# Optimization experiments

Hardware: AMD Instinct MI355X
Metric: run time of the kernel (lower is better)

## Reference

```python
import jax, jax.numpy as jnp
import numpy as np

N, E, IN, H, C = 50000, 800000, 256, 4, 64  # nodes, edges, input_dim, heads, hidden_dim


def setup_inputs() -> dict:
    key = jax.random.key(0)
    ks = jax.random.split(key, 12)
    rn = lambda k, shp, s: jax.random.normal(k, shp, jnp.float32) * s
    glorot = lambda fi, fo: (2.0 / (fi + fo)) ** 0.5
    return {
        "x": rn(ks[0], (N, IN), 1.0),
        "edge_index": jax.random.randint(ks[1], (2, E), 0, N, dtype=jnp.int32),
        # gat1: in=IN, out=H*C, concat=True
        "W1": rn(ks[2], (IN, H * C), glorot(IN, H * C)),
        "att_src1": rn(ks[3], (H, C), 0.1),
        "att_dst1": rn(ks[4], (H, C), 0.1),
        "b1": jnp.zeros((H * C,), jnp.float32),
        # gat2: in=H*C, out=C, heads=1, concat=False
        "W2": rn(ks[5], (H * C, C), glorot(H * C, C)),
        "att_src2": rn(ks[6], (1, C), 0.1),
        "att_dst2": rn(ks[7], (1, C), 0.1),
        "b2": jnp.zeros((C,), jnp.float32),
        # attention pooling head + entity scorer
        "att_w": rn(ks[8], (C, 1), 0.1),
        "att_b": jnp.zeros((1,), jnp.float32),
        "fc_w": rn(ks[9], (C, 1), 0.1),
        "fc_b": jnp.zeros((1,), jnp.float32),
    }


def _gat_conv(x, src, dst, W, a_src, a_dst, bias, concat):
    """PyG GATConv (self-loops already appended to src/dst)."""
    n = x.shape[0]
    heads, ch = a_src.shape
    h = (x @ W).reshape(n, heads, ch)                      # [N,H,C]
    s = jnp.sum(h * a_src[None], axis=-1)                  # [N,H]
    d = jnp.sum(h * a_dst[None], axis=-1)                  # [N,H]
    e = jax.nn.leaky_relu(s[src] + d[dst], 0.2)            # [Etot,H]
    # segment softmax over incoming edges of each dst node
    m = jax.ops.segment_max(e, dst, num_segments=n)        # [N,H]
    m = jnp.where(jnp.isfinite(m), m, 0.0)
    ex = jnp.exp(e - m[dst])
    den = jax.ops.segment_sum(ex, dst, num_segments=n)
    alpha = ex / den[dst]                                  # [Etot,H]
    out = jax.ops.segment_sum(h[src] * alpha[:, :, None], dst, num_segments=n)  # [N,H,C]
    out = out.reshape(n, heads * ch) if concat else out.mean(axis=1)
    return out + bias


def reference(x, edge_index, W1, att_src1, att_dst1, b1, W2, att_src2, att_dst2, b2,
              att_w, att_b, fc_w, fc_b):
    n = x.shape[0]
    loop = jnp.arange(n, dtype=edge_index.dtype)           # add_self_loops=True
    src = jnp.concatenate([edge_index[0], loop])
    dst = jnp.concatenate([edge_index[1], loop])
    h = jax.nn.relu(_gat_conv(x, src, dst, W1, att_src1, att_dst1, b1, True))   # [N,H*C]
    h = jax.nn.relu(_gat_conv(h, src, dst, W2, att_src2, att_dst2, b2, False))  # [N,C]
    aw = jax.nn.softmax(h @ att_w + att_b, axis=0)         # softmax over all nodes, [N,1]
    global_rep = jnp.sum(aw * h, axis=0)                   # [C]
    entity_probs = jax.nn.sigmoid(h @ fc_w + fc_b).squeeze(-1)  # [N]
    return entity_probs, global_rep
```

## Files before the change

### kernel.cpp

```cpp
#include <hip/hip_runtime.h>
#include <hip/hip_bf16.h>
#include <math.h>

#define N_NODES 50000
#define N_EDGES 800000
#define ETOT    850000
#define IN_DIM  256
#define HC      256
#define HEADS   4
#define CD      64

typedef __bf16    bf16x8 __attribute__((ext_vector_type(8)));
typedef float     f32x4  __attribute__((ext_vector_type(4)));
typedef _Float16  f16x4  __attribute__((ext_vector_type(4)));

static __device__ __forceinline__ float lrelu(float x) { return x > 0.f ? x : 0.2f * x; }

static __device__ __forceinline__ unsigned short bf16_rne(float f) {
    union { float f; unsigned u; } c; c.f = f;
    unsigned u = c.u;
    return (unsigned short)((u + 0x7FFFu + ((u >> 16) & 1u)) >> 16);
}
static __device__ __forceinline__ float bf16_to_f(unsigned short h) {
    union { unsigned u; float f; } c; c.u = ((unsigned)h) << 16;
    return c.f;
}

__global__ void k_init(int* counts, int* cursor,
                       float* s1, float* d1, float* s2, float* d2) {
    int i = blockIdx.x * 256 + threadIdx.x;
    if (i < N_NODES) {
        counts[i] = 1; cursor[i] = 0;
        float4 z = {0.f, 0.f, 0.f, 0.f};
        reinterpret_cast<float4*>(s1)[i] = z;
        reinterpret_cast<float4*>(d1)[i] = z;
        s2[i] = 0.f; d2[i] = 0.f;
    }
}

__global__ void k_degree(const int* __restrict__ dst, int* __restrict__ counts) {
    int i = blockIdx.x * 256 + threadIdx.x;
    if (i < N_EDGES) atomicAdd(&counts[dst[i]], 1);
}

__global__ __launch_bounds__(1024) void k_scan_a(const int* __restrict__ counts,
                                                 int* __restrict__ rowptr,
                                                 int* __restrict__ bsum) {
    __shared__ int sd[1024];
    int t = threadIdx.x;
    int i = blockIdx.x * 1024 + t;
    int v = (i < N_NODES) ? counts[i] : 0;
    sd[t] = v; __syncthreads();
    for (int off = 1; off < 1024; off <<= 1) {
        int add = (t >= off) ? sd[t - off] : 0;
        __syncthreads();
        sd[t] += add;
        __syncthreads();
    }
    if (i < N_NODES) rowptr[i + 1] = sd[t];
    if (t == 1023) bsum[blockIdx.x] = sd[1023];
    if (i == 0) rowptr[0] = 0;
}

__global__ void k_scan_b(int* bsum, int nb) {
    if (threadIdx.x == 0) {
        int run = 0;
        for (int b = 0; b < nb; ++b) { int t = bsum[b]; bsum[b] = run; run += t; }
    }
}

__global__ void k_scan_c(int* __restrict__ rowptr, const int* __restrict__ bsum) {
    int i = blockIdx.x * 256 + threadIdx.x;
    if (i < N_NODES) rowptr[i + 1] += bsum[i >> 10];
}

__global__ void k_scatter(const int* __restrict__ src, const int* __restrict__ dst,
                          const int* __restrict__ rowptr, int* __restrict__ cursor,
                          int* __restrict__ src_sorted) {
    int i = blockIdx.x * 256 + threadIdx.x;
    if (i >= ETOT) return;
    int s, d;
    if (i < N_EDGES) { s = src[i]; d = dst[i]; }
    else             { s = i - N_EDGES; d = s; }
    int pos = rowptr[d] + atomicAdd(&cursor[d], 1);
    src_sorted[pos] = s;
}

__global__ void k_convx(const float* __restrict__ x,
                        unsigned short* __restrict__ hi,
                        unsigned short* __restrict__ lo) {
    int i = blockIdx.x * 256 + threadIdx.x;
    if (i >= N_NODES * IN_DIM / 4) return;
    float4 v = reinterpret_cast<const float4*>(x)[i];
    ushort4 h, l;
    h.x = bf16_rne(v.x); l.x = bf16_rne(v.x - bf16_to_f(h.x));
    h.y = bf16_rne(v.y); l.y = bf16_rne(v.y - bf16_to_f(h.y));
    h.z = bf16_rne(v.z); l.z = bf16_rne(v.z - bf16_to_f(h.z));
    h.w = bf16_rne(v.w); l.w = bf16_rne(v.w - bf16_to_f(h.w));
    reinterpret_cast<ushort4*>(hi)[i] = h;
    reinterpret_cast<ushort4*>(lo)[i] = l;
}

__global__ void k_convw(const float* __restrict__ W,
                        unsigned short* __restrict__ hiT,
                        unsigned short* __restrict__ loT, int Nc) {
    int idx = blockIdx.x * 256 + threadIdx.x;
    if (idx >= Nc * 256) return;
    int n = idx >> 8, k = idx & 255;
    float v = W[(size_t)k * Nc + n];
    unsigned short h = bf16_rne(v);
    hiT[idx] = h;
    loT[idx] = bf16_rne(v - bf16_to_f(h));
}

__global__ __launch_bounds__(256) void k_gemm_f(
    const unsigned short* __restrict__ Ahi, const unsigned short* __restrict__ Alo,
    const unsigned short* __restrict__ BThi, const unsigned short* __restrict__ BTlo,
    _Float16* __restrict__ Of16,
    float* __restrict__ s_out, float* __restrict__ d_out,
    const float* __restrict__ a_s, const float* __restrict__ a_d,
    int M, int Nc)
{
    __shared__ unsigned short lA[2][128 * 64];
    __shared__ unsigned short lB[2][64 * 64];
    const int t = threadIdx.x;
    const int lane = t & 63, w = t >> 6;
    const int wr = w >> 1, wc = w & 1;
    const int row0 = blockIdx.y * 128;
    const int col0 = blockIdx.x * 64;
    const int hs = Nc >> 6;

    f32x4 acc[4][2];
    const f32x4 fzero = {0.f, 0.f, 0.f, 0.f};
    #pragma unroll
    for (int m = 0; m < 4; ++m)
        #pragma unroll
        for (int n = 0; n < 2; ++n) acc[m][n] = fzero;

    for (int k0 = 0; k0 < 256; k0 += 64) {
        for (int i = t; i < 1024; i += 256) {
            int r = i >> 3, c = i & 7;
            int gr = row0 + r; if (gr >= M) gr = M - 1;
            uint4 vhi = *reinterpret_cast<const uint4*>(Ahi + (size_t)gr * 256 + k0 + c * 8);
            uint4 vlo = *reinterpret_cast<const uint4*>(Alo + (size_t)gr * 256 + k0 + c * 8);
            unsigned bo = (unsigned)(r * 128 + c * 16) ^ ((r & 7) << 4);
            *reinterpret_cast<uint4*>((char*)lA[0] + bo) = vhi;
            *reinterpret_cast<uint4*>((char*)lA[1] + bo) = vlo;
        }
        for (int i = t; i < 512; i += 256) {
            int r = i >> 3, c = i & 7;
            uint4 vhi = *reinterpret_cast<const uint4*>(BThi + (size_t)(col0 + r) * 256 + k0 + c * 8);
            uint4 vlo = *reinterpret_cast<const uint4*>(BTlo + (size_t)(col0 + r) * 256 + k0 + c * 8);
            unsigned bo = (unsigned)(r * 128 + c * 16) ^ ((r & 7) << 4);
            *reinterpret_cast<uint4*>((char*)lB[0] + bo) = vhi;
            *reinterpret_cast<uint4*>((char*)lB[1] + bo) = vlo;
        }
        __syncthreads();
        #pragma unroll
        for (int ks = 0; ks < 2; ++ks) {
            const int kb = ks * 64 + (lane >> 4) * 16;
            bf16x8 ah[4], al[4], bh[2], bl[2];
            #pragma unroll
            for (int m = 0; m < 4; ++m) {
                int r = wr * 64 + m * 16 + (lane & 15);
                unsigned bo = (unsigned)(r * 128 + kb) ^ ((r & 7) << 4);
                ah[m] = *reinterpret_cast<const bf16x8*>((char*)lA[0] + bo);
                al[m] = *reinterpret_cast<const bf16x8*>((char*)lA[1] + bo);
            }
            #pragma unroll
            for (int n = 0; n < 2; ++n) {
                int r = wc * 32 + n * 16 + (lane & 15);
                unsigned bo = (unsigned)(r * 128 + kb) ^ ((r & 7) << 4);
                bh[n] = *reinterpret_cast<const bf16x8*>((char*)lB[0] + bo);
                bl[n] = *reinterpret_cast<const bf16x8*>((char*)lB[1] + bo);
            }
            #pragma unroll
            for (int m = 0; m < 4; ++m)
                #pragma unroll
                for (int n = 0; n < 2; ++n) {
                    acc[m][n] = __builtin_amdgcn_mfma_f32_16x16x32_bf16(ah[m], bh[n], acc[m][n], 0, 0, 0);
                    acc[m][n] = __builtin_amdgcn_mfma_f32_16x16x32_bf16(ah[m], bl[n], acc[m][n], 0, 0, 0);
                    acc[m][n] = __builtin_amdgcn_mfma_f32_16x16x32_bf16(al[m], bh[n], acc[m][n], 0, 0, 0);
                }
        }
        __syncthreads();
    }
    const int cll = wc * 32 + (lane & 15);
    const float as0 = a_s[col0 + cll], as1 = a_s[col0 + cll + 16];
    const float ad0 = a_d[col0 + cll], ad1 = a_d[col0 + cll + 16];
    #pragma unroll
    for (int m = 0; m < 4; ++m) {
        #pragma unroll
        for (int r = 0; r < 4; ++r) {
            int row = row0 + wr * 64 + m * 16 + (lane >> 4) * 4 + r;
            float v0 = acc[m][0][r], v1 = acc[m][1][r];
            float sp = v0 * as0 + v1 * as1;
            float dp = v0 * ad0 + v1 * ad1;
            #pragma unroll
            for (int off = 1; off < 16; off <<= 1) {
                sp += __shfl_xor(sp, off, 64);
                dp += __shfl_xor(dp, off, 64);
            }
            if (row < M) {
                Of16[(size_t)row * Nc + col0 + cll]      = (_Float16)v0;
                Of16[(size_t)row * Nc + col0 + cll + 16] = (_Float16)v1;
                if ((lane & 15) == 0) {
                    atomicAdd(&s_out[(size_t)row * hs + blockIdx.x], sp);
                    atomicAdd(&d_out[(size_t)row * hs + blockIdx.x], dp);
                }
            }
        }
    }
}

__global__ __launch_bounds__(256) void k_agg1(const int* __restrict__ rowptr,
                                              const int* __restrict__ srcs,
                                              const _Float16* __restrict__ h1f,
                                              const float* __restrict__ s1,
                                              const float* __restrict__ d1,
                                              const float* __restrict__ b1,
                                              unsigned short* __restrict__ o_hi,
                                              unsigned short* __restrict__ o_lo) {
    const int w = threadIdx.x >> 6, l = threadIdx.x & 63;
    const int v = blockIdx.x * 4 + w;
    if (v >= N_NODES) return;
    __shared__ float exs[4][64][4];
    __shared__ int   us[4][64];
    const int row0 = rowptr[v], row1 = rowptr[v + 1];
    const float4 dv = *reinterpret_cast<const float4*>(d1 + 4 * v);
    const int head = l >> 4;
    float a0 = 0.f, a1 = 0.f, a2 = 0.f, a3 = 0.f, den = 0.f;

    for (int c0 = row0; c0 < row1; c0 += 64) {
        const int nc = min(64, row1 - c0);
        if (l < nc) {
            int u = srcs[c0 + l];
            float4 s = *reinterpret_cast<const float4*>(s1 + 4 * u);
            us[w][l] = u;
            exs[w][l][0] = __expf(lrelu(s.x + dv.x));
            exs[w][l][1] = __expf(lrelu(s.y + dv.y));
            exs[w][l][2] = __expf(lrelu(s.z + dv.z));
            exs[w][l][3] = __expf(lrelu(s.w + dv.w));
        }
        __builtin_amdgcn_wave_barrier();
        for (int j = 0; j < nc; ++j) {
            int u = us[w][j];
            float ex = exs[w][j][head];
            f16x4 hv = *reinterpret_cast<const f16x4*>(h1f + (size_t)u * 256 + l * 4);
            a0 += ex * (float)hv[0];
            a1 += ex * (float)hv[1];
            a2 += ex * (float)hv[2];
            a3 += ex * (float)hv[3];
            den += ex;
        }
        __builtin_amdgcn_wave_barrier();
    }
    const float4 bb = *reinterpret_cast<const float4*>(b1 + l * 4);
    float o0 = fmaxf(a0 / den + bb.x, 0.f);
    float o1 = fmaxf(a1 / den + bb.y, 0.f);
    float o2 = fmaxf(a2 / den + bb.z, 0.f);
    float o3 = fmaxf(a3 / den + bb.w, 0.f);
    ushort4 h4, l4;
    h4.x = bf16_rne(o0); l4.x = bf16_rne(o0 - bf16_to_f(h4.x));
    h4.y = bf16_rne(o1); l4.y = bf16_rne(o1 - bf16_to_f(h4.y));
    h4.z = bf16_rne(o2); l4.z = bf16_rne(o2 - bf16_to_f(h4.z));
    h4.w = bf16_rne(o3); l4.w = bf16_rne(o3 - bf16_to_f(h4.w));
    *reinterpret_cast<ushort4*>(o_hi + (size_t)v * 256 + l * 4) = h4;
    *reinterpret_cast<ushort4*>(o_lo + (size_t)v * 256 + l * 4) = l4;
}

__global__ __launch_bounds__(256) void k_agg2(const int* __restrict__ rowptr,
                                              const int* __restrict__ srcs,
                                              const _Float16* __restrict__ t2f,
                                              const float* __restrict__ s2,
                                              const float* __restrict__ d2,
                                              const float* __restrict__ b2,
                                              float* __restrict__ h2) {
    const int w = threadIdx.x >> 6, l = threadIdx.x & 63;
    const int v = blockIdx.x * 4 + w;
    if (v >= N_NODES) return;
    __shared__ float exw[4][64];
    __shared__ int   uw[4][64];
    const int row0 = rowptr[v], row1 = rowptr[v + 1];
    const float dvv = d2[v];
    float acc = 0.f, den = 0.f;
    for (int c0 = row0; c0 < row1; c0 += 64) {
        int nc = min(64, row1 - c0);
        if (l < nc) {
            int u = srcs[c0 + l];
            uw[w][l] = u;
            exw[w][l] = __expf(lrelu(s2[u] + dvv));
        }
        __builtin_amdgcn_wave_barrier();
        for (int j = 0; j < nc; ++j) {
            int u = uw[w][j];
            float ex = exw[w][j];
            acc += ex * (float)t2f[(size_t)u * CD + l];
            den += ex;
        }
        __builtin_amdgcn_wave_barrier();
    }
    h2[(size_t)v * CD + l] = fmaxf(acc / den + b2[l], 0.f);
}

__global__ __launch_bounds__(256) void k_head(const float* __restrict__ h2,
                                              const float* __restrict__ att_w,
                                              const float* __restrict__ att_b,
                                              const float* __restrict__ fc_w,
                                              const float* __restrict__ fc_b,
                                              float* __restrict__ logit,
                                              float* __restrict__ outp) {
    int wave = threadIdx.x >> 6, lane = threadIdx.x & 63;
    int v = blockIdx.x * 4 + wave;
    if (v >= N_NODES) return;
    float hv = h2[(size_t)v * CD + lane];
    float a = hv * att_w[lane];
    float f = hv * fc_w[lane];
    #pragma unroll
    for (int off = 32; off; off >>= 1) {
        a += __shfl_down(a, off, 64);
        f += __shfl_down(f, off, 64);
    }
    if (lane == 0) {
        logit[v] = a + att_b[0];
        float z = f + fc_b[0];
        outp[v] = 1.f / (1.f + __expf(-z));
    }
}

__global__ __launch_bounds__(256) void k_pmax(const float* __restrict__ logit,
                                              float* __restrict__ pmax) {
    __shared__ float sd[256];
    int t = threadIdx.x;
    float lm = -1e30f;
    for (int i = blockIdx.x * 256 + t; i < N_NODES; i += gridDim.x * 256)
        lm = fmaxf(lm, logit[i]);
    sd[t] = lm; __syncthreads();
    for (int s = 128; s; s >>= 1) { if (t < s) sd[t] = fmaxf(sd[t], sd[t + s]); __syncthreads(); }
    if (t == 0) pmax[blockIdx.x] = sd[0];
}

__global__ __launch_bounds__(256) void k_finmax(const float* __restrict__ pmax,
                                                float* __restrict__ gmax,
                                                float* __restrict__ gsum,
                                                float* __restrict__ gvec) {
    __shared__ float sd[256];
    int t = threadIdx.x;
    sd[t] = pmax[t];
    __syncthreads();
    for (int s = 128; s; s >>= 1) { if (t < s) sd[t] = fmaxf(sd[t], sd[t + s]); __syncthreads(); }
    if (t == 0) { *gmax = sd[0]; *gsum = 0.f; }
    if (t < 64) gvec[t] = 0.f;
}

__global__ __launch_bounds__(256) void k_pool(const float* __restrict__ h2,
                                              const float* __restrict__ logit,
                                              const float* __restrict__ gmax,
                                              float* __restrict__ gsum,
                                              float* __restrict__ gvec) {
    int wave = threadIdx.x >> 6, lane = threadIdx.x & 63;
    __shared__ float acc_s[4][64];
    __shared__ float ws_s[4];
    float m = *gmax;
    float acc = 0.f, wsum = 0.f;
    int gw = blockIdx.x * 4 + wave;
    int nw = gridDim.x * 4;
    for (int v = gw; v < N_NODES; v += nw) {
        float w = __expf(logit[v] - m);
        acc += w * h2[(size_t)v * CD + lane];
        if (lane == 0) wsum += w;
    }
    acc_s[wave][lane] = acc;
    if (lane == 0) ws_s[wave] = wsum;
    __syncthreads();
    if (threadIdx.x < 64) {
        float a = acc_s[0][threadIdx.x] + acc_s[1][threadIdx.x] +
                  acc_s[2][threadIdx.x] + acc_s[3][threadIdx.x];
        atomicAdd(&gvec[threadIdx.x], a);
    }
    if (threadIdx.x == 0)
        atomicAdd(gsum, ws_s[0] + ws_s[1] + ws_s[2] + ws_s[3]);
}

__global__ void k_writeout(const float* __restrict__ gvec,
                           const float* __restrict__ gsum,
                           float* __restrict__ outg) {
    int t = threadIdx.x;
    if (t < 64) outg[t] = gvec[t] / *gsum;
}

extern "C" void kernel_launch(void* const* d_in, const int* in_sizes, int n_in,
                              void* d_out, int out_size, void* d_ws, size_t ws_size,
                              hipStream_t stream) {
    const float* x    = (const float*)d_in[0];
    const int*   ei   = (const int*)d_in[1];
    const float* W1   = (const float*)d_in[2];
    const float* as1  = (const float*)d_in[3];
    const float* ad1  = (const float*)d_in[4];
    const float* b1   = (const float*)d_in[5];
    const float* W2   = (const float*)d_in[6];
    const float* as2  = (const float*)d_in[7];
    const float* ad2  = (const float*)d_in[8];
    const float* b2   = (const float*)d_in[9];
    const float* attw = (const float*)d_in[10];
    const float* attb = (const float*)d_in[11];
    const float* fcw  = (const float*)d_in[12];
    const float* fcb  = (const float*)d_in[13];
    const int* srcE = ei;
    const int* dstE = ei + N_EDGES;

    char* ws = (char*)d_ws;
    size_t off = 0;
    auto take = [&](size_t bytes) -> void* {
        void* p = ws + off;
        off += (bytes + 255) & ~(size_t)255;
        return p;
    };
    _Float16* h1f  = (_Float16*)take((size_t)N_NODES * HC * 2);
    _Float16* t2f  = (_Float16*)take((size_t)N_NODES * CD * 2);
    float* h2   = (float*)take((size_t)N_NODES * CD * 4);
    float* s1   = (float*)take((size_t)N_NODES * 4 * 4);
    float* d1   = (float*)take((size_t)N_NODES * 4 * 4);
    float* s2   = (float*)take((size_t)N_NODES * 4);
    float* d2   = (float*)take((size_t)N_NODES * 4);
    int* counts = (int*)take((size_t)N_NODES * 4);
    int* cursor = (int*)take((size_t)N_NODES * 4);
    int* rowptr = (int*)take((size_t)(N_NODES + 1) * 4);
    int* bsum   = (int*)take(64 * 4);
    int* src_sorted = (int*)take((size_t)ETOT * 4);
    unsigned short* xhi = (unsigned short*)take((size_t)N_NODES * IN_DIM * 2);
    unsigned short* xlo = (unsigned short*)take((size_t)N_NODES * IN_DIM * 2);
    unsigned short* W1Thi = (unsigned short*)take(256 * 256 * 2);
    unsigned short* W1Tlo = (unsigned short*)take(256 * 256 * 2);
    unsigned short* W2Thi = (unsigned short*)take(64 * 256 * 2);
    unsigned short* W2Tlo = (unsigned short*)take(64 * 256 * 2);
    float* logit = (float*)take((size_t)N_NODES * 4);
    float* pmax  = (float*)take(256 * 4);
    float* gmax  = (float*)take(4);
    float* gsum  = (float*)take(4);
    float* gvec  = (float*)take(64 * 4);
    unsigned short* out1hi = xhi;
    unsigned short* out1lo = xlo;

    k_init<<<(N_NODES + 255) / 256, 256, 0, stream>>>(counts, cursor, s1, d1, s2, d2);
    k_degree<<<(N_EDGES + 255) / 256, 256, 0, stream>>>(dstE, counts);
    int nb = (N_NODES + 1023) / 1024;
    k_scan_a<<<nb, 1024, 0, stream>>>(counts, rowptr, bsum);
    k_scan_b<<<1, 64, 0, stream>>>(bsum, nb);
    k_scan_c<<<(N_NODES + 255) / 256, 256, 0, stream>>>(rowptr, bsum);
    k_scatter<<<(ETOT + 255) / 256, 256, 0, stream>>>(srcE, dstE, rowptr, cursor, src_sorted);

    k_convx<<<(N_NODES * IN_DIM / 4 + 255) / 256, 256, 0, stream>>>(x, xhi, xlo);
    k_convw<<<(256 * 256 + 255) / 256, 256, 0, stream>>>(W1, W1Thi, W1Tlo, HC);
    k_convw<<<(64 * 256 + 255) / 256, 256, 0, stream>>>(W2, W2Thi, W2Tlo, CD);

    k_gemm_f<<<dim3(HC / 64, (N_NODES + 127) / 128), 256, 0, stream>>>(
        xhi, xlo, W1Thi, W1Tlo, h1f, s1, d1, as1, ad1, N_NODES, HC);
    k_agg1<<<(N_NODES + 3) / 4, 256, 0, stream>>>(rowptr, src_sorted, h1f, s1, d1, b1, out1hi, out1lo);

    k_gemm_f<<<dim3(CD / 64, (N_NODES + 127) / 128), 256, 0, stream>>>(
        out1hi, out1lo, W2Thi, W2Tlo, t2f, s2, d2, as2, ad2, N_NODES, CD);
    k_agg2<<<(N_NODES + 3) / 4, 256, 0, stream>>>(rowptr, src_sorted, t2f, s2, d2, b2, h2);

    k_head<<<(N_NODES + 3) / 4, 256, 0, stream>>>(h2, attw, attb, fcw, fcb, logit, (float*)d_out);
    k_pmax<<<256, 256, 0, stream>>>(logit, pmax);
    k_finmax<<<1, 256, 0, stream>>>(pmax, gmax, gsum, gvec);
    k_pool<<<256, 256, 0, stream>>>(h2, logit, gmax, gsum, gvec);
    k_writeout<<<1, 64, 0, stream>>>(gvec, gsum, (float*)d_out + N_NODES);
}
```

Baseline: 437.9 us.

## Replace LDS-tiled split-bf16 GEMM with register-direct loads and full-head wave tiles

The GEMM drops LDS staging and barriers. Each wave now loads its MFMA operands straight from global memory and owns a 64x64 tile, which covers a whole attention head. Because one wave sees all 64 columns of a head, the per-head score dot products are finished inside the wave and written with plain stores instead of atomics, so the zero-init of the s/d buffers is removed from k_init. The cost is that operand reuse now depends on L1/L2 caching rather than shared memory, and the global loads are strided across rows.

Result: faster. 428.1 us (-2.2%).

```diff
diff --git a/kernel.cpp b/kernel.cpp
--- a/kernel.cpp
+++ b/kernel.cpp
@@ -26,16 +26,9 @@
     return c.f;
 }
 
-__global__ void k_init(int* counts, int* cursor,
-                       float* s1, float* d1, float* s2, float* d2) {
+__global__ void k_init(int* counts, int* cursor) {
     int i = blockIdx.x * 256 + threadIdx.x;
-    if (i < N_NODES) {
-        counts[i] = 1; cursor[i] = 0;
-        float4 z = {0.f, 0.f, 0.f, 0.f};
-        reinterpret_cast<float4*>(s1)[i] = z;
-        reinterpret_cast<float4*>(d1)[i] = z;
-        s2[i] = 0.f; d2[i] = 0.f;
-    }
+    if (i < N_NODES) { counts[i] = 1; cursor[i] = 0; }
 }
 
 __global__ void k_degree(const int* __restrict__ dst, int* __restrict__ counts) {
@@ -113,7 +106,7 @@
     loT[idx] = bf16_rne(v - bf16_to_f(h));
 }
 
-__global__ __launch_bounds__(256) void k_gemm_f(
+__global__ __launch_bounds__(256) void k_gemm_r(
     const unsigned short* __restrict__ Ahi, const unsigned short* __restrict__ Alo,
     const unsigned short* __restrict__ BThi, const unsigned short* __restrict__ BTlo,
     _Float16* __restrict__ Of16,
@@ -121,92 +114,82 @@
     const float* __restrict__ a_s, const float* __restrict__ a_d,
     int M, int Nc)
 {
-    __shared__ unsigned short lA[2][128 * 64];
-    __shared__ unsigned short lB[2][64 * 64];
-    const int t = threadIdx.x;
-    const int lane = t & 63, w = t >> 6;
-    const int wr = w >> 1, wc = w & 1;
-    const int row0 = blockIdx.y * 128;
+    const int lane = threadIdx.x & 63, w = threadIdx.x >> 6;
+    const int row0 = blockIdx.y * 256 + w * 64;
     const int col0 = blockIdx.x * 64;
     const int hs = Nc >> 6;
-
-    f32x4 acc[4][2];
+    const int rl = lane & 15, kg = lane >> 4;
+
+    f32x4 acc[4][4];
     const f32x4 fzero = {0.f, 0.f, 0.f, 0.f};
     #pragma unroll
     for (int m = 0; m < 4; ++m)
         #pragma unroll
-        for (int n = 0; n < 2; ++n) acc[m][n] = fzero;
-
-    for (int k0 = 0; k0 < 256; k0 += 64) {
-        for (int i = t; i < 1024; i += 256) {
-            int r = i >> 3, c = i & 7;
-            int gr = row0 + r; if (gr >= M) gr = M - 1;
-            uint4 vhi = *reinterpret_cast<const uint4*>(Ahi + (size_t)gr * 256 + k0 + c * 8);
-            uint4 vlo = *reinterpret_cast<const uint4*>(Alo + (size_t)gr * 256 + k0 + c * 8);
-            unsigned bo = (unsigned)(r * 128 + c * 16) ^ ((r & 7) << 4);
-            *reinterpret_cast<uint4*>((char*)lA[0] + bo) = vhi;
-            *reinterpret_cast<uint4*>((char*)lA[1] + bo) = vlo;
-        }
-        for (int i = t; i < 512; i += 256) {
-            int r = i >> 3, c = i & 7;
-            uint4 vhi = *reinterpret_cast<const uint4*>(BThi + (size_t)(col0 + r) * 256 + k0 + c * 8);
-            uint4 vlo = *reinterpret_cast<const uint4*>(BTlo + (size_t)(col0 + r) * 256 + k0 + c * 8);
-            unsigned bo = (unsigned)(r * 128 + c * 16) ^ ((r & 7) << 4);
-            *reinterpret_cast<uint4*>((char*)lB[0] + bo) = vhi;
-            *reinterpret_cast<uint4*>((char*)lB[1] + bo) = vlo;
-        }
-        __syncthreads();
+        for (int n = 0; n < 4; ++n) acc[m][n] = fzero;
+
+    size_t aoff[4], boff[4];
+    #pragma unroll
+    for (int m = 0; m < 4; ++m) {
+        int r = row0 + m * 16 + rl; if (r >= M) r = M - 1;
+        aoff[m] = (size_t)r * 256 + kg * 8;
+    }
+    #pragma unroll
+    for (int n = 0; n < 4; ++n) {
+        int c = col0 + n * 16 + rl;
+        boff[n] = (size_t)c * 256 + kg * 8;
+    }
+
+    #pragma unroll 2
+    for (int k0 = 0; k0 < 256; k0 += 32) {
+        bf16x8 ah[4], al[4], bh[4], bl[4];
         #pragma unroll
-        for (int ks = 0; ks < 2; ++ks) {
-            const int kb = ks * 64 + (lane >> 4) * 16;
-            bf16x8 ah[4], al[4], bh[2], bl[2];
+        for (int m = 0; m < 4; ++m) {
+            ah[m] = *reinterpret_cast<const bf16x8*>(Ahi + aoff[m] + k0);
+            al[m] = *reinterpret_cast<const bf16x8*>(Alo + aoff[m] + k0);
+        }
+        #pragma unroll
+        for (int n = 0; n < 4; ++n) {
+            bh[n] = *reinterpret_cast<const bf16x8*>(BThi + boff[n] + k0);
+            bl[n] = *reinterpret_cast<const bf16x8*>(BTlo + boff[n] + k0);
+        }
+        #pragma unroll
+        for (int m = 0; m < 4; ++m)
             #pragma unroll
-            for (int m = 0; m < 4; ++m) {
-                int r = wr * 64 + m * 16 + (lane & 15);
-                unsigned bo = (unsigned)(r * 128 + kb) ^ ((r & 7) << 4);
-                ah[m] = *reinterpret_cast<const bf16x8*>((char*)lA[0] + bo);
-                al[m] = *reinterpret_cast<const bf16x8*>((char*)lA[1] + bo);
+            for (int n = 0; n < 4; ++n) {
+                acc[m][n] = __builtin_amdgcn_mfma_f32_16x16x32_bf16(ah[m], bh[n], acc[m][n], 0, 0, 0);
+                acc[m][n] = __builtin_amdgcn_mfma_f32_16x16x32_bf16(ah[m], bl[n], acc[m][n], 0, 0, 0);
+                acc[m][n] = __builtin_amdgcn_mfma_f32_16x16x32_bf16(al[m], bh[n], acc[m][n], 0, 0, 0);
             }
-            #pragma unroll
-            for (int n = 0; n < 2; ++n) {
-                int r = wc * 32 + n * 16 + (lane & 15);
-                unsigned bo = (unsigned)(r * 128 + kb) ^ ((r & 7) << 4);
-                bh[n] = *reinterpret_cast<const bf16x8*>((char*)lB[0] + bo);
-                bl[n] = *reinterpret_cast<const bf16x8*>((char*)lB[1] + bo);
-            }
-            #pragma unroll
-            for (int m = 0; m < 4; ++m)
-                #pragma unroll
-                for (int n = 0; n < 2; ++n) {
-                    acc[m][n] = __builtin_amdgcn_mfma_f32_16x16x32_bf16(ah[m], bh[n], acc[m][n], 0, 0, 0);
-                    acc[m][n] = __builtin_amdgcn_mfma_f32_16x16x32_bf16(ah[m], bl[n], acc[m][n], 0, 0, 0);
-                    acc[m][n] = __builtin_amdgcn_mfma_f32_16x16x32_bf16(al[m], bh[n], acc[m][n], 0, 0, 0);
-                }
-        }
-        __syncthreads();
-    }
-    const int cll = wc * 32 + (lane & 15);
-    const float as0 = a_s[col0 + cll], as1 = a_s[col0 + cll + 16];
-    const float ad0 = a_d[col0 + cll], ad1 = a_d[col0 + cll + 16];
+    }
+
+    float as_[4], ad_[4];
+    #pragma unroll
+    for (int n = 0; n < 4; ++n) {
+        as_[n] = a_s[col0 + n * 16 + rl];
+        ad_[n] = a_d[col0 + n * 16 + rl];
+    }
     #pragma unroll
     for (int m = 0; m < 4; ++m) {
         #pragma unroll
         for (int r = 0; r < 4; ++r) {
-            int row = row0 + wr * 64 + m * 16 + (lane >> 4) * 4 + r;
-            float v0 = acc[m][0][r], v1 = acc[m][1][r];
-            float sp = v0 * as0 + v1 * as1;
-            float dp = v0 * ad0 + v1 * ad1;
+            int row = row0 + m * 16 + kg * 4 + r;
+            float v0 = acc[m][0][r], v1 = acc[m][1][r], v2 = acc[m][2][r], v3 = acc[m][3][r];
+            float sp = v0 * as_[0] + v1 * as_[1] + v2 * as_[2] + v3 * as_[3];
+            float dp = v0 * ad_[0] + v1 * ad_[1] + v2 * ad_[2] + v3 * ad_[3];
             #pragma unroll
             for (int off = 1; off < 16; off <<= 1) {
                 sp += __shfl_xor(sp, off, 64);
                 dp += __shfl_xor(dp, off, 64);
             }
             if (row < M) {
-                Of16[(size_t)row * Nc + col0 + cll]      = (_Float16)v0;
-                Of16[(size_t)row * Nc + col0 + cll + 16] = (_Float16)v1;
-                if ((lane & 15) == 0) {
-                    atomicAdd(&s_out[(size_t)row * hs + blockIdx.x], sp);
-                    atomicAdd(&d_out[(size_t)row * hs + blockIdx.x], dp);
+                _Float16* o = Of16 + (size_t)row * Nc + col0 + rl;
+                o[0]  = (_Float16)v0;
+                o[16] = (_Float16)v1;
+                o[32] = (_Float16)v2;
+                o[48] = (_Float16)v3;
+                if (rl == 0) {
+                    s_out[(size_t)row * hs + blockIdx.x] = sp;
+                    d_out[(size_t)row * hs + blockIdx.x] = dp;
                 }
             }
         }
@@ -442,7 +425,7 @@
     unsigned short* out1hi = xhi;
     unsigned short* out1lo = xlo;
 
-    k_init<<<(N_NODES + 255) / 256, 256, 0, stream>>>(counts, cursor, s1, d1, s2, d2);
+    k_init<<<(N_NODES + 255) / 256, 256, 0, stream>>>(counts, cursor);
     k_degree<<<(N_EDGES + 255) / 256, 256, 0, stream>>>(dstE, counts);
     int nb = (N_NODES + 1023) / 1024;
     k_scan_a<<<nb, 1024, 0, stream>>>(counts, rowptr, bsum);
@@ -454,11 +437,11 @@
     k_convw<<<(256 * 256 + 255) / 256, 256, 0, stream>>>(W1, W1Thi, W1Tlo, HC);
     k_convw<<<(64 * 256 + 255) / 256, 256, 0, stream>>>(W2, W2Thi, W2Tlo, CD);
 
-    k_gemm_f<<<dim3(HC / 64, (N_NODES + 127) / 128), 256, 0, stream>>>(
+    k_gemm_r<<<dim3(HC / 64, (N_NODES + 255) / 256), 256, 0, stream>>>(
         xhi, xlo, W1Thi, W1Tlo, h1f, s1, d1, as1, ad1, N_NODES, HC);
     k_agg1<<<(N_NODES + 3) / 4, 256, 0, stream>>>(rowptr, src_sorted, h1f, s1, d1, b1, out1hi, out1lo);
 
-    k_gemm_f<<<dim3(CD / 64, (N_NODES + 127) / 128), 256, 0, stream>>>(
+    k_gemm_r<<<dim3(CD / 64, (N_NODES + 255) / 256), 256, 0, stream>>>(
         out1hi, out1lo, W2Thi, W2Tlo, t2f, s2, d2, as2, ad2, N_NODES, CD);
     k_agg2<<<(N_NODES + 3) / 4, 256, 0, stream>>>(rowptr, src_sorted, t2f, s2, d2, b2, h2);
 
```
